# Performance work log

Hardware: AMD Instinct MI355X
Metric: run time of the kernel (lower is better)

## Reference

```python
import jax, jax.numpy as jnp
import numpy as np

B, R, C, D = 8, 64, 16, 128  # batch, num_rows(taxa), patch_num, embed_dim


def _linear_init(key, fan_in, fan_out):
    lim = 1.0 / np.sqrt(fan_in)
    kw, kb = jax.random.split(key)
    W = jax.random.uniform(kw, (fan_in, fan_out), jnp.float32, -lim, lim)
    b = jax.random.uniform(kb, (fan_out,), jnp.float32, -lim, lim)
    return W, b


def setup_inputs() -> dict:
    key = jax.random.key(0)
    ks = jax.random.split(key, 8)
    row_np, col_np = np.triu_indices(R, k=1)  # n = R*(R-1)/2 = 2016 pairs
    hW, hb = _linear_init(ks[1], D, D)
    gW, gb = _linear_init(ks[2], D, D)
    qW, qb = _linear_init(ks[3], D, D)
    kW, kb = _linear_init(ks[4], D, D)
    s1W, s1b = _linear_init(ks[5], D, D)
    s2W, s2b = _linear_init(ks[6], D, 1)
    return {
        "batch_input": jax.random.normal(ks[0], (B, R, C, D), jnp.float32),
        "seq_mask": jnp.ones((B, 1, C), jnp.float32),
        "row": jnp.asarray(row_np, jnp.int32),
        "col": jnp.asarray(col_np, jnp.int32),
        "hW": hW, "hb": hb, "gW": gW, "gb": gb,
        "qW": qW, "qb": qb, "kW": kW, "kb": kb,
        "s1W": s1W, "s1b": s1b, "s2W": s2W, "s2b": s2b,
    }


def reference(batch_input, seq_mask, row, col,
              hW, hb, gW, gb, qW, qb, kW, kb, s1W, s1b, s2W, s2b):
    b, r, c, d = batch_input.shape
    n = row.shape[0]
    # pairwise gather: x_i, x_j -> [b, n, c, d]
    x_i = batch_input[:, row]
    x_j = batch_input[:, col]
    # sigmoid gate fusion of the pair
    h = (x_i - x_j) @ hW + hb
    z = jax.nn.sigmoid(h)
    x = z * x_i + (1.0 - z) * x_j
    # masked global attention over the batch_input 'memory' (r > 2 branch)
    q = x @ qW + qb                    # [b, n, c, d]
    k = batch_input @ kW + kb          # [b, r, c, d]
    scale = 1.0 / np.sqrt(d * c).astype(np.float32)
    alpha = jnp.einsum('bncd,brcd->bnr', q, k) * scale
    # -inf at (pair n, rows row[n] and col[n]); equivalent to += -inf on finite scores
    neg_mask = (jnp.zeros((n, r), bool)
                .at[jnp.arange(n), row].set(True)
                .at[jnp.arange(n), col].set(True))
    alpha = jnp.where(neg_mask[None], -jnp.inf, alpha)
    alpha = jax.nn.softmax(alpha, axis=-1)
    x_glob = jnp.einsum('bnr,brcd->bncd', alpha, batch_input)
    g = x_glob @ gW + gb
    w = jax.nn.sigmoid(g)
    x = (1.0 - w) * x + w * x_glob
    # s_out: Linear -> GELU(exact) -> Linear(d,1), then mask and reduce over c
    s = jax.nn.gelu(x @ s1W + s1b, approximate=False) @ s2W + s2b  # [b, n, c, 1]
    scores = s[..., 0] * seq_mask       # seq_mask [b,1,c] broadcasts over n
    return scores.sum(-1)               # [b, n]
```

## Files before the change

kernel.cpp:

```cpp
#include <hip/hip_runtime.h>
#include <hip/hip_bf16.h>
#include <math.h>

#define B_    8
#define R_    64
#define C_    16
#define D_    128
#define NPAIR 2016
#define CD    2048
#define PG    16
#define NPG   126
#define XSTR  136
#define NEG_BIG (-1e30f)
#define SCALE 0.022097086912079608f

typedef __attribute__((ext_vector_type(8))) short short8;
typedef __attribute__((ext_vector_type(4))) float float4v;

#define WMH  0u
#define WML  16384u
#define WHH  32768u
#define WHL  49152u
#define WGH  65536u
#define WGL  81920u
#define WSH  98304u
#define VECO 131072u
#define QBKO 131592u
#define MO   132616u
#define XTO  1181192u
#define GTO  2229768u
#define HO   3278344u

__device__ __forceinline__ unsigned short f2b(float f){
    union { float f; unsigned int u; } v; v.f = f;
    const unsigned int r = v.u + 0x7FFFu + ((v.u >> 16) & 1u);
    return (unsigned short)(r >> 16);
}
__device__ __forceinline__ float b2f(unsigned short u){
    union { unsigned int i; float f; } v; v.i = ((unsigned int)u) << 16; return v.f;
}
__device__ __forceinline__ float lo2f(unsigned int u){
    union { unsigned int i; float f; } v; v.i = u << 16; return v.f;
}
__device__ __forceinline__ float hif2f(unsigned int u){
    union { unsigned int i; float f; } v; v.i = u & 0xffff0000u; return v.f;
}
__device__ __forceinline__ unsigned int pack2(float a, float b){
    return (unsigned int)f2b(a) | ((unsigned int)f2b(b) << 16);
}
__device__ __forceinline__ void split_bf(float v, float* hi, float* lo){
    union { float f; unsigned int u; } x; x.f = v;
    const unsigned int r = (x.u + 0x7FFFu + ((x.u >> 16) & 1u)) & 0xffff0000u;
    union { unsigned int u; float f; } h; h.u = r;
    *hi = h.f; *lo = v - h.f;
}
__device__ __forceinline__ float sigmoid_safe(float x){
    x = fminf(fmaxf(x, -30.f), 30.f);
    return 1.f / (1.f + __expf(-x));
}
__device__ __forceinline__ float gelu_tanh(float x){
    const float u = x*x;
    const float g2 = x*(1.5957691216057308f + 0.07135481627159f*u);
    return x * sigmoid_safe(g2);
}

__global__ __launch_bounds__(256) void k_prepA(
    const float* __restrict__ x,
    const float* __restrict__ hW, const float* __restrict__ gW,
    const float* __restrict__ qW, const float* __restrict__ qb,
    const float* __restrict__ kW, const float* __restrict__ kb,
    unsigned short* __restrict__ ws)
{
    __shared__ __align__(16) unsigned short tile[128*69];
    const int bid = blockIdx.x, t = threadIdx.x;
    if (bid < 64){
        __shared__ float sKW[2][128];
        const int e0 = bid*2;
        sKW[t>>7][t&127] = kW[(e0 + (t>>7))*128 + (t&127)];
        __syncthreads();
        const int e = t>>7, d = t&127;
        const float* qr = qW + d*128;
        const float* kr = sKW[e];
        float acc = 0.f;
        #pragma unroll 8
        for (int g = 0; g < 128; g += 4){
            const float4 qv = *reinterpret_cast<const float4*>(qr + g);
            acc += qv.x*kr[g] + qv.y*kr[g+1] + qv.z*kr[g+2] + qv.w*kr[g+3];
        }
        float hi, lo; split_bf(acc, &hi, &lo);
        ws[WMH + d*128 + (e0+e)] = f2b(hi);
        ws[WML + d*128 + (e0+e)] = f2b(lo);
    } else if (bid == 64){
        float* vec = (float*)(ws + VECO);
        if (t < 128){
            float a1 = 0.f, a2 = 0.f;
            #pragma unroll 8
            for (int g = 0; g < 128; g += 4){
                const float4 q4 = *reinterpret_cast<const float4*>(qW + t*128 + g);
                const float4 k4 = *reinterpret_cast<const float4*>(kW + t*128 + g);
                const float4 kb4 = *reinterpret_cast<const float4*>(kb + g);
                const float4 qb4 = *reinterpret_cast<const float4*>(qb + g);
                a1 += q4.x*kb4.x + q4.y*kb4.y + q4.z*kb4.z + q4.w*kb4.w;
                a2 += k4.x*qb4.x + k4.y*qb4.y + k4.z*qb4.z + k4.w*qb4.w;
            }
            vec[t] = a1;
            vec[128 + t] = a2;
        } else if (t == 128){
            float a = 0.f;
            for (int g = 0; g < 128; ++g) a = fmaf(qb[g], kb[g], a);
            vec[256] = a;
        }
    } else if (bid < 193){
        const int j = bid - 65;
        const int mat = j >> 6;
        const int gid = (j & 63)*256 + t;
        const int n = gid >> 7, k = gid & 127;
        const float* W = (mat==0) ? hW : gW;
        const unsigned int baseh = (mat==0) ? WHH : WGH;
        const unsigned int basel = (mat==0) ? WHL : WGL;
        float hi, lo; split_bf(W[k*128 + n], &hi, &lo);
        ws[baseh + gid] = f2b(hi);
        ws[basel + gid] = f2b(lo);
    } else {
        const int blk = bid - 193;
        const int b = blk >> 4, cd0 = (blk & 15)*128;
        #pragma unroll
        for (int i = 0; i < 32; ++i){
            const int idx = i*256 + t;
            const int r = idx >> 7, cc = idx & 127;
            tile[cc*69 + r] = f2b(x[((size_t)(b*64 + r))*CD + cd0 + cc]);
        }
        __syncthreads();
        const unsigned int base = XTO + (unsigned int)(b*2048 + cd0)*64;
        #pragma unroll
        for (int j = 0; j < 32; ++j){
            const int idx = j*256 + t;
            const int cc = idx >> 6, r = idx & 63;
            ws[base + cc*64 + r] = tile[cc*69 + r];
        }
    }
}

__global__ __launch_bounds__(512) void k_prepB(const float* __restrict__ x,
        const float* __restrict__ gb, const float* __restrict__ s1W,
        unsigned short* __restrict__ ws)
{
    __shared__ __align__(16) unsigned short smem[8832];
    __shared__ float sQ[4];
    const int bid = blockIdx.x, t = threadIdx.x;
    const int w = t >> 6, lane = t & 63, l15 = lane & 15, quad = lane >> 4;

    if (bid < 256){
        const bool isM = (bid >= 128);
        unsigned short* sH = smem;
        const int br0 = (bid & 127) * 4;
        const float* kqf = (const float*)(ws + VECO) + 128;
        const float* mbf = (const float*)(ws + VECO);
        if (t < 4) sQ[t] = 0.f;
        __syncthreads();
        #pragma unroll
        for (int i = 0; i < 4; ++i){
            const int flat = (t + 512*i)*4;
            const int lr = flat >> 11, cd = flat & 2047;
            const float4 v = *reinterpret_cast<const float4*>(x + (size_t)(br0+lr)*CD + cd);
            const int ad = (lr*16 + (cd>>7))*XSTR + lr*8 + (cd & 127);
            uint2 uh;
            uh.x = pack2(v.x, v.y); uh.y = pack2(v.z, v.w);
            *reinterpret_cast<uint2*>(sH + ad) = uh;
            if (isM){
                const float4 kq4 = *reinterpret_cast<const float4*>(kqf + (cd & 127));
                atomicAdd(&sQ[lr], v.x*kq4.x + v.y*kq4.y + v.z*kq4.z + v.w*kq4.w);
            }
        }
        __syncthreads();
        const unsigned short* Bh = isM ? (ws+WMH) : (ws+WHH);
        const unsigned short* Bl = isM ? (ws+WML) : (ws+WHL);
        const float bv = isM ? mbf[w*16 + l15] : 0.f;
        float4v acc[4];
        #pragma unroll
        for (int mt = 0; mt < 4; ++mt){ float4v d = {bv,bv,bv,bv}; acc[mt] = d; }
        #pragma unroll
        for (int ks = 0; ks < 4; ++ks){
            const int ko = ks*32 + quad*8;
            const int bd = (w*16 + l15)*128 + ko;
            const short8 bh = *reinterpret_cast<const short8*>(Bh + bd);
            const short8 bl = *reinterpret_cast<const short8*>(Bl + bd);
            #pragma unroll
            for (int mt = 0; mt < 4; ++mt){
                const int ad = (mt*16 + l15)*XSTR + mt*8 + ko;
                const short8 ah = *reinterpret_cast<const short8*>(sH + ad);
                float4v d = acc[mt];
                d = __builtin_amdgcn_mfma_f32_16x16x32_bf16(ah, bh, d, 0,0,0);
                d = __builtin_amdgcn_mfma_f32_16x16x32_bf16(ah, bl, d, 0,0,0);
                acc[mt] = d;
            }
        }
        const int f = w*16 + l15;
        const unsigned int dsto = isM ? MO : HO;
        #pragma unroll
        for (int mt = 0; mt < 4; ++mt)
        #pragma unroll
        for (int e = 0; e < 4; ++e){
            const int c = quad*4 + e;
            ws[dsto + (size_t)(br0+mt)*CD + c*128 + f] = f2b(acc[mt][e]);
        }
        if (isM && t < 4){
            const float s0 = ((const float*)(ws + VECO))[256];
            ((float*)(ws + QBKO))[br0 + t] = sQ[t] + 16.f*s0;
        }
    } else if (bid < 384){
        unsigned short* tileB = smem;
        const int gidx = bid - 256;
        const int b = gidx >> 4, cd0 = (gidx & 15)*128;
        #pragma unroll
        for (int i = 0; i < 16; ++i){
            const int idx = i*512 + t;
            const int r = idx >> 7, dd = idx & 127;
            tileB[r*138 + dd] = f2b(x[(size_t)(b*64 + r)*CD + cd0 + dd]);
        }
        __syncthreads();
        float4v acc[4];
        #pragma unroll
        for (int nt = 0; nt < 4; ++nt){ float4v z = {0.f,0.f,0.f,0.f}; acc[nt] = z; }
        #pragma unroll
        for (int ks = 0; ks < 4; ++ks){
            const int ko = ks*32 + quad*8;
            const int adg = (w*16 + l15)*128 + ko;
            const short8 ah = *reinterpret_cast<const short8*>(ws + WGH + adg);
            const short8 al = *reinterpret_cast<const short8*>(ws + WGL + adg);
            #pragma unroll
            for (int nt = 0; nt < 4; ++nt){
                const short8 bb = *reinterpret_cast<const short8*>(tileB + (nt*16 + l15)*138 + ko);
                float4v d = acc[nt];
                d = __builtin_amdgcn_mfma_f32_16x16x32_bf16(ah, bb, d, 0,0,0);
                d = __builtin_amdgcn_mfma_f32_16x16x32_bf16(al, bb, d, 0,0,0);
                acc[nt] = d;
            }
        }
        #pragma unroll
        for (int nt = 0; nt < 4; ++nt)
        #pragma unroll
        for (int e = 0; e < 4; ++e){
            const int f = w*16 + quad*4 + e;
            const float val = acc[nt][e] + gb[f];
            ws[GTO + (size_t)(b*2048 + cd0 + f)*64 + nt*16 + l15] = f2b(val);
        }
    } else {
        const int gid = (bid - 384)*4096 + t;
        #pragma unroll
        for (int i = 0; i < 8; ++i){
            const int g = gid + i*512;
            const int n = g >> 7, k = g & 127;
            ws[WSH + g] = f2b(s1W[k*128 + n]);
        }
    }
}

__global__ __launch_bounds__(512, 4) void k_main(
    const float* __restrict__ x, const float* __restrict__ seq_mask,
    const int* __restrict__ row, const int* __restrict__ col,
    const float* __restrict__ hb, const float* __restrict__ s1b,
    const float* __restrict__ s2W, const float* __restrict__ s2b,
    const unsigned short* __restrict__ ws, float* __restrict__ out)
{
    __shared__ __align__(16) unsigned short sX[256*XSTR + 128];
    __shared__ __align__(16) unsigned short sAl[16*72];
    __shared__ float sLog[1024];
    __shared__ float sOut[PG];
    __shared__ float sMask[16];
    __shared__ int srp[PG], scp[PG];

    const int t = threadIdx.x;
    const int w = t >> 6, lane = t & 63, l15 = lane & 15, quad = lane >> 4;
    const int b = blockIdx.x, p0 = blockIdx.y * PG;
    const float* xb = x + (size_t)b * R_ * CD;
    const unsigned short* Hb = ws + HO + (size_t)b * R_ * CD;

    if (t < PG){ srp[t] = row[p0+t]; scp[t] = col[p0+t]; sOut[t] = 0.f; }
    if (t >= 32 && t < 48) sMask[t-32] = seq_mask[b*C_ + (t-32)];
    for (int i = t; i < 1152; i += 512) sAl[i] = 0;
    for (int i = t; i < 1024; i += 512) sLog[i] = 0.f;
    __syncthreads();

    #pragma unroll 4
    for (int i = 0; i < 16; ++i){
        const int flat = (t + 512*i)*4;
        const int p = flat >> 11, cd = flat & 2047;
        const int ri = srp[p], ci = scp[p];
        const float4 xi = *reinterpret_cast<const float4*>(xb + (size_t)ri*CD + cd);
        const float4 xj = *reinterpret_cast<const float4*>(xb + (size_t)ci*CD + cd);
        const uint2 Hi2 = *reinterpret_cast<const uint2*>(Hb + (size_t)ri*CD + cd);
        const uint2 Hj2 = *reinterpret_cast<const uint2*>(Hb + (size_t)ci*CD + cd);
        const float4 h4 = *reinterpret_cast<const float4*>(hb + (cd & 127));
        const float z0 = sigmoid_safe(lo2f(Hi2.x)  - lo2f(Hj2.x)  + h4.x);
        const float z1 = sigmoid_safe(hif2f(Hi2.x) - hif2f(Hj2.x) + h4.y);
        const float z2 = sigmoid_safe(lo2f(Hi2.y)  - lo2f(Hj2.y)  + h4.z);
        const float z3 = sigmoid_safe(hif2f(Hi2.y) - hif2f(Hj2.y) + h4.w);
        const float v0 = xj.x + z0*(xi.x - xj.x);
        const float v1 = xj.y + z1*(xi.y - xj.y);
        const float v2 = xj.z + z2*(xi.z - xj.z);
        const float v3 = xj.w + z3*(xi.w - xj.w);
        const int ad = (p*16 + (cd>>7))*XSTR + p*8 + (cd & 127);
        uint2 uv; uv.x = pack2(v0,v1); uv.y = pack2(v2,v3);
        *reinterpret_cast<uint2*>(sX + ad) = uv;
    }
    __syncthreads();

    {
        const int rt = w & 3, kh = w >> 2;
        const int r = rt*16 + l15;
        const unsigned short* Mr = ws + MO + ((size_t)b*64 + r)*CD + kh*1024;
        float4v d = {0.f,0.f,0.f,0.f};
        #pragma unroll 8
        for (int ks = 0; ks < 32; ++ks){
            const int k = kh*1024 + ks*32 + quad*8;
            const short8 ah = *reinterpret_cast<const short8*>(
                sX + (l15*16 + (k>>7))*XSTR + l15*8 + (k & 127));
            const short8 bh = *reinterpret_cast<const short8*>(Mr + ks*32 + quad*8);
            d = __builtin_amdgcn_mfma_f32_16x16x32_bf16(ah, bh, d, 0,0,0);
        }
        #pragma unroll
        for (int e = 0; e < 4; ++e){
            const int pp = quad*4 + e;
            atomicAdd(&sLog[pp*64 + r], d[e]);
        }
    }
    __syncthreads();

    if (t < 256){
        const int pp = t >> 4, l = t & 15;
        const int ri = srp[pp], ci = scp[pp];
        const float* qbk = (const float*)(ws + QBKO);
        float v[4]; float m = NEG_BIG;
        #pragma unroll
        for (int k = 0; k < 4; ++k){
            const int r = l + 16*k;
            float lv = (sLog[pp*64 + r] + qbk[b*64 + r]) * SCALE;
            if (r == ri || r == ci) lv = NEG_BIG;
            v[k] = lv; m = fmaxf(m, lv);
        }
        #pragma unroll
        for (int s = 1; s < 16; s <<= 1) m = fmaxf(m, __shfl_xor(m, s));
        float e4[4]; float sum = 0.f;
        #pragma unroll
        for (int k = 0; k < 4; ++k){
            const int r = l + 16*k;
            const bool masked = (r == ri || r == ci);
            const float e = masked ? 0.f : __expf(fmaxf(v[k]-m, -80.f));
            e4[k] = e; sum += e;
        }
        #pragma unroll
        for (int s = 1; s < 16; s <<= 1) sum += __shfl_xor(sum, s);
        const float inv = 1.f / sum;
        #pragma unroll
        for (int k = 0; k < 4; ++k) sAl[pp*72 + l + 16*k] = f2b(e4[k]*inv);
    }
    __syncthreads();

    {
        const unsigned short* XTb = ws + XTO + (size_t)b * CD * 64;
        const unsigned short* GTb = ws + GTO + (size_t)b * CD * 64;
        const short8 Ah0 = *reinterpret_cast<const short8*>(sAl + l15*72 + quad*8);
        const short8 Ah1 = *reinterpret_cast<const short8*>(sAl + l15*72 + 32 + quad*8);
        #pragma unroll 4
        for (int j = 0; j < 16; ++j){
            const int cd = w*256 + j*16 + l15;
            const short8 xb0 = *reinterpret_cast<const short8*>(XTb + (size_t)cd*64 + quad*8);
            const short8 xb1 = *reinterpret_cast<const short8*>(XTb + (size_t)cd*64 + 32 + quad*8);
            const short8 gb0 = *reinterpret_cast<const short8*>(GTb + (size_t)cd*64 + quad*8);
            const short8 gb1 = *reinterpret_cast<const short8*>(GTb + (size_t)cd*64 + 32 + quad*8);
            float4v dx = {0.f,0.f,0.f,0.f}, dg = {0.f,0.f,0.f,0.f};
            dx = __builtin_amdgcn_mfma_f32_16x16x32_bf16(Ah0, xb0, dx, 0,0,0);
            dx = __builtin_amdgcn_mfma_f32_16x16x32_bf16(Ah1, xb1, dx, 0,0,0);
            dg = __builtin_amdgcn_mfma_f32_16x16x32_bf16(Ah0, gb0, dg, 0,0,0);
            dg = __builtin_amdgcn_mfma_f32_16x16x32_bf16(Ah1, gb1, dg, 0,0,0);
            #pragma unroll
            for (int e = 0; e < 4; ++e){
                const int pp = quad*4 + e;
                const int ad = (pp*16 + (cd>>7))*XSTR + pp*8 + (cd & 127);
                const float wv = sigmoid_safe(dg[e]);
                const float xo = b2f(sX[ad]);
                sX[ad] = f2b((1.f - wv)*xo + wv*dx[e]);
            }
        }
    }
    __syncthreads();

    {
        float4v acc16[16];
        const float bv = s1b[w*16 + l15];
        #pragma unroll
        for (int mt = 0; mt < 16; ++mt){ float4v d = {bv,bv,bv,bv}; acc16[mt] = d; }
        #pragma unroll
        for (int ks = 0; ks < 4; ++ks){
            const int ko = ks*32 + quad*8;
            const int bd = (w*16 + l15)*128 + ko;
            const short8 bh = *reinterpret_cast<const short8*>(ws + WSH + bd);
            #pragma unroll
            for (int mt = 0; mt < 16; ++mt){
                const short8 a = *reinterpret_cast<const short8*>(sX + (mt*16 + l15)*XSTR + mt*8 + ko);
                acc16[mt] = __builtin_amdgcn_mfma_f32_16x16x32_bf16(a, bh, acc16[mt], 0,0,0);
            }
        }
        const float s2v = s2W[w*16 + l15];
        const float mk0 = sMask[quad*4+0], mk1 = sMask[quad*4+1];
        const float mk2 = sMask[quad*4+2], mk3 = sMask[quad*4+3];
        float psum[16];
        #pragma unroll
        for (int mt = 0; mt < 16; ++mt){
            float s = gelu_tanh(acc16[mt][0]) * mk0;
            s += gelu_tanh(acc16[mt][1]) * mk1;
            s += gelu_tanh(acc16[mt][2]) * mk2;
            s += gelu_tanh(acc16[mt][3]) * mk3;
            psum[mt] = s * s2v;
        }
        #pragma unroll
        for (int s = 1; s < 64; s <<= 1)
            #pragma unroll
            for (int mt = 0; mt < 16; ++mt) psum[mt] += __shfl_xor(psum[mt], s);
        if (lane == 0){
            #pragma unroll
            for (int mt = 0; mt < 16; ++mt) atomicAdd(&sOut[mt], psum[mt]);
        }
    }
    __syncthreads();

    if (t < PG){
        float msum = 0.f;
        #pragma unroll
        for (int c = 0; c < 16; ++c) msum += sMask[c];
        out[(size_t)b*NPAIR + p0 + t] = sOut[t] + s2b[0]*msum;
    }
}

extern "C" void kernel_launch(void* const* d_in, const int* in_sizes, int n_in,
                              void* d_out, int out_size, void* d_ws, size_t ws_size,
                              hipStream_t stream)
{
    const float* x    = (const float*)d_in[0];
    const float* mask = (const float*)d_in[1];
    const int*   row  = (const int*)d_in[2];
    const int*   col  = (const int*)d_in[3];
    const float* hW  = (const float*)d_in[4];  const float* hb  = (const float*)d_in[5];
    const float* gW  = (const float*)d_in[6];  const float* gb  = (const float*)d_in[7];
    const float* qW  = (const float*)d_in[8];  const float* qb  = (const float*)d_in[9];
    const float* kW  = (const float*)d_in[10]; const float* kb  = (const float*)d_in[11];
    const float* s1W = (const float*)d_in[12]; const float* s1b = (const float*)d_in[13];
    const float* s2W = (const float*)d_in[14]; const float* s2b = (const float*)d_in[15];

    unsigned short* ws = (unsigned short*)d_ws;

    k_prepA<<<321, 256, 0, stream>>>(x, hW, gW, qW, qb, kW, kb, ws);
    k_prepB<<<388, 512, 0, stream>>>(x, gb, s1W, ws);
    k_main<<<dim3(B_, NPG), 512, 0, stream>>>(x, mask, row, col,
                                              hb, s1b, s2W, s2b,
                                              ws, (float*)d_out);
}
```

Baseline: 236.8 us.

## Use hardware bf16 pack, fast rcp sigmoid, wave-reduced atomics, padded logit stride

Swaps the software round-to-nearest bf16 conversion for the v_cvt_pk_bf16_f32 instruction. Replaces the clamped sigmoid and the softmax division with the hardware reciprocal. Replaces per-thread shared-memory atomics in prepB with a wavefront shuffle reduction followed by one atomic per wave. Pads the sLog row stride to 68 to reduce LDS bank conflicts. Dropping the clamp risks inf/NaN edge behaviour, and rcp is lower precision than a true divide.

```diff
diff --git a/kernel.cpp b/kernel.cpp
--- a/kernel.cpp
+++ b/kernel.cpp
@@ -11,6 +11,7 @@
 #define PG    16
 #define NPG   126
 #define XSTR  136
+#define LSTR  68
 #define NEG_BIG (-1e30f)
 #define SCALE 0.022097086912079608f
 
@@ -46,7 +47,14 @@
     union { unsigned int i; float f; } v; v.i = u & 0xffff0000u; return v.f;
 }
 __device__ __forceinline__ unsigned int pack2(float a, float b){
-    return (unsigned int)f2b(a) | ((unsigned int)f2b(b) << 16);
+    unsigned int r;
+    asm("v_cvt_pk_bf16_f32 %0, %1, %2" : "=v"(r) : "v"(a), "v"(b));
+    return r;
+}
+__device__ __forceinline__ unsigned short f2b1(float a){
+    unsigned int r;
+    asm("v_cvt_pk_bf16_f32 %0, %1, %1" : "=v"(r) : "v"(a));
+    return (unsigned short)r;
 }
 __device__ __forceinline__ void split_bf(float v, float* hi, float* lo){
     union { float f; unsigned int u; } x; x.f = v;
@@ -55,8 +63,7 @@
     *hi = h.f; *lo = v - h.f;
 }
 __device__ __forceinline__ float sigmoid_safe(float x){
-    x = fminf(fmaxf(x, -30.f), 30.f);
-    return 1.f / (1.f + __expf(-x));
+    return __builtin_amdgcn_rcpf(1.f + __expf(-x));
 }
 __device__ __forceinline__ float gelu_tanh(float x){
     const float u = x*x;
@@ -158,10 +165,12 @@
         const float* mbf = (const float*)(ws + VECO);
         if (t < 4) sQ[t] = 0.f;
         __syncthreads();
+        float qacc[4] = {0.f, 0.f, 0.f, 0.f};
         #pragma unroll
         for (int i = 0; i < 4; ++i){
             const int flat = (t + 512*i)*4;
-            const int lr = flat >> 11, cd = flat & 2047;
+            const int lr = i;
+            const int cd = flat & 2047;
             const float4 v = *reinterpret_cast<const float4*>(x + (size_t)(br0+lr)*CD + cd);
             const int ad = (lr*16 + (cd>>7))*XSTR + lr*8 + (cd & 127);
             uint2 uh;
@@ -169,7 +178,16 @@
             *reinterpret_cast<uint2*>(sH + ad) = uh;
             if (isM){
                 const float4 kq4 = *reinterpret_cast<const float4*>(kqf + (cd & 127));
-                atomicAdd(&sQ[lr], v.x*kq4.x + v.y*kq4.y + v.z*kq4.z + v.w*kq4.w);
+                qacc[i] = v.x*kq4.x + v.y*kq4.y + v.z*kq4.z + v.w*kq4.w;
+            }
+        }
+        if (isM){
+            #pragma unroll
+            for (int i = 0; i < 4; ++i){
+                float s = qacc[i];
+                #pragma unroll
+                for (int off = 1; off < 64; off <<= 1) s += __shfl_xor(s, off);
+                if (lane == 0) atomicAdd(&sQ[i], s);
             }
         }
         __syncthreads();
@@ -265,7 +283,7 @@
 {
     __shared__ __align__(16) unsigned short sX[256*XSTR + 128];
     __shared__ __align__(16) unsigned short sAl[16*72];
-    __shared__ float sLog[1024];
+    __shared__ float sLog[16*LSTR];
     __shared__ float sOut[PG];
     __shared__ float sMask[16];
     __shared__ int srp[PG], scp[PG];
@@ -279,7 +297,7 @@
     if (t < PG){ srp[t] = row[p0+t]; scp[t] = col[p0+t]; sOut[t] = 0.f; }
     if (t >= 32 && t < 48) sMask[t-32] = seq_mask[b*C_ + (t-32)];
     for (int i = t; i < 1152; i += 512) sAl[i] = 0;
-    for (int i = t; i < 1024; i += 512) sLog[i] = 0.f;
+    for (int i = t; i < 16*LSTR; i += 512) sLog[i] = 0.f;
     __syncthreads();
 
     #pragma unroll 4
@@ -322,7 +340,7 @@
         #pragma unroll
         for (int e = 0; e < 4; ++e){
             const int pp = quad*4 + e;
-            atomicAdd(&sLog[pp*64 + r], d[e]);
+            atomicAdd(&sLog[pp*LSTR + r], d[e]);
         }
     }
     __syncthreads();
@@ -335,7 +353,7 @@
         #pragma unroll
         for (int k = 0; k < 4; ++k){
             const int r = l + 16*k;
-            float lv = (sLog[pp*64 + r] + qbk[b*64 + r]) * SCALE;
+            float lv = (sLog[pp*LSTR + r] + qbk[b*64 + r]) * SCALE;
             if (r == ri || r == ci) lv = NEG_BIG;
             v[k] = lv; m = fmaxf(m, lv);
         }
@@ -351,9 +369,9 @@
         }
         #pragma unroll
         for (int s = 1; s < 16; s <<= 1) sum += __shfl_xor(sum, s);
-        const float inv = 1.f / sum;
-        #pragma unroll
-        for (int k = 0; k < 4; ++k) sAl[pp*72 + l + 16*k] = f2b(e4[k]*inv);
+        const float inv = __builtin_amdgcn_rcpf(sum);
+        #pragma unroll
+        for (int k = 0; k < 4; ++k) sAl[pp*72 + l + 16*k] = f2b1(e4[k]*inv);
     }
     __syncthreads();
 
@@ -380,7 +398,7 @@
                 const int ad = (pp*16 + (cd>>7))*XSTR + pp*8 + (cd & 127);
                 const float wv = sigmoid_safe(dg[e]);
                 const float xo = b2f(sX[ad]);
-                sX[ad] = f2b((1.f - wv)*xo + wv*dx[e]);
+                sX[ad] = f2b1((1.f - wv)*xo + wv*dx[e]);
             }
         }
     }
```

Measured after the change: 228.5 us. 3.5% less time.
